# Performance work log

Hardware: AMD Instinct MI355X
Metric: run time of the kernel (lower is better)

## Reference

```python
import jax, jax.numpy as jnp
import numpy as np


def _pairwise_sqdist(a, b):
    # a: [B,N,2], b: [B,M,2] -> [B,N,M] squared Euclidean distances
    a2 = jnp.sum(a * a, axis=-1)  # [B,N]
    b2 = jnp.sum(b * b, axis=-1)  # [B,M]
    ab = jnp.einsum('bnd,bmd->bnm', a, b)  # [B,N,M]
    return a2[:, :, None] + b2[:, None, :] - 2.0 * ab


def setup_inputs() -> dict:
    key = jax.random.key(0)
    k1, k2 = jax.random.split(key)
    B, N, M, D = 16, 2048, 2048, 2
    preds = jax.random.normal(k1, (B, N, D), dtype=jnp.float32)
    targs = jax.random.normal(k2, (B, M, D), dtype=jnp.float32)
    subcoef = jnp.ones((D,), dtype=jnp.float32)
    return {"preds": preds, "targs": targs, "subcoef": subcoef}


def reference(preds, targs, subcoef):
    # Bidirectional Chamfer-style NN L1 loss, faithful to NNLoss.nn_loss.
    d2 = _pairwise_sqdist(preds, targs)  # [B,N,M]

    # preds -> nearest GT (KDTree over targs queried with preds)
    nn_t = jnp.argmin(d2, axis=2)  # [B,N]
    matched_t = jnp.take_along_axis(targs, nn_t[:, :, None], axis=1)  # [B,N,2]
    move_preds_to_gt = jnp.sum(jnp.abs(preds - matched_t) * subcoef)

    # targs -> nearest pred (KDTree over preds queried with targs)
    nn_p = jnp.argmin(d2, axis=1)  # [B,M]
    matched_p = jnp.take_along_axis(preds, nn_p[:, :, None], axis=1)  # [B,M,2]
    move_gts_to_pred = jnp.sum(jnp.abs(matched_p - targs))

    return move_gts_to_pred + move_preds_to_gt
```

## Files before the change

kernel.cpp:

```cpp
#include <hip/hip_runtime.h>


typedef float v2f __attribute__((ext_vector_type(2)));
typedef float v4f __attribute__((ext_vector_type(4)));

constexpr int B      = 16;
constexpr int NPTS   = 2048;
constexpr int BLK    = 1024;
constexpr int G      = 256;
constexpr int S      = 16;
constexpr int QPT    = 4;
constexpr int SEGLEN = NPTS / S;
constexpr int QUADS  = SEGLEN / 4;
constexpr int NBLK   = 2 * B * (NPTS / G);

__global__ __launch_bounds__(BLK) void nn_main(
    const float* __restrict__ preds, const float* __restrict__ targs,
    const float* __restrict__ subcoef, float* __restrict__ out)
{
    __shared__ v4f xs4[NPTS / 4];
    __shared__ v4f ys4[NPTS / 4];
    __shared__ unsigned long long cand[S * G];
    __shared__ float ssum[BLK / 64];

    const int blk  = blockIdx.x;
    const int dir  = blk >> 7;
    const int b    = (blk >> 3) & 15;
    const int tile = blk & 7;

    const float2* qb = reinterpret_cast<const float2*>(dir == 0 ? preds : targs)
                       + b * NPTS + tile * G;
    const float2* db = reinterpret_cast<const float2*>(dir == 0 ? targs : preds)
                       + b * NPTS;

    const float4* db4 = reinterpret_cast<const float4*>(db);
    {
        const int j = threadIdx.x & 511;
        const float4 a = db4[2 * j];
        const float4 c = db4[2 * j + 1];
        if (threadIdx.x < 512) xs4[j] = {a.x, a.z, c.x, c.z};
        else                   ys4[j] = {a.y, a.w, c.y, c.w};
    }

    const int qslot = threadIdx.x & 63;
    const int seg   = threadIdx.x >> 6;

    v2f   m2x[QPT], m2y[QPT];
    float best[QPT];
    int   bj[QPT];
    #pragma unroll
    for (int q = 0; q < QPT; ++q) {
        const float2 qp = qb[qslot + q * 64];
        const float ax = -2.0f * qp.x, ay = -2.0f * qp.y;
        m2x[q] = {ax, ax};
        m2y[q] = {ay, ay};
        best[q] = 3.402823466e+38f;
        bj[q] = 0;
    }
    __syncthreads();

    const v4f* xsp = xs4 + seg * QUADS;
    const v4f* ysp = ys4 + seg * QUADS;
    #pragma unroll 8
    for (int i = 0; i < QUADS; ++i) {
        const v4f X = xsp[i];
        const v4f Y = ysp[i];
        const v2f xa = {X.x, X.y}, xb = {X.z, X.w};
        const v2f ya = {Y.x, Y.y}, yb = {Y.z, Y.w};
        const v2f t2a = __builtin_elementwise_fma(xa, xa, ya * ya);
        const v2f t2b = __builtin_elementwise_fma(xb, xb, yb * yb);
        #pragma unroll
        for (int q = 0; q < QPT; ++q) {
            const v2f da = __builtin_elementwise_fma(
                m2x[q], xa, __builtin_elementwise_fma(m2y[q], ya, t2a));
            const v2f dc = __builtin_elementwise_fma(
                m2x[q], xb, __builtin_elementwise_fma(m2y[q], yb, t2b));
            const v2f m2 = __builtin_elementwise_min(da, dc);
            const float dm = fminf(m2.x, m2.y);
            if (dm < best[q]) { best[q] = dm; bj[q] = i; }
        }
    }

    #pragma unroll
    for (int q = 0; q < QPT; ++q) {
        const v4f X = xsp[bj[q]];
        const v4f Y = ysp[bj[q]];
        const v2f xa = {X.x, X.y}, xb = {X.z, X.w};
        const v2f ya = {Y.x, Y.y}, yb = {Y.z, Y.w};
        const v2f t2a = __builtin_elementwise_fma(xa, xa, ya * ya);
        const v2f t2b = __builtin_elementwise_fma(xb, xb, yb * yb);
        const v2f da = __builtin_elementwise_fma(
            m2x[q], xa, __builtin_elementwise_fma(m2y[q], ya, t2a));
        const v2f dc = __builtin_elementwise_fma(
            m2x[q], xb, __builtin_elementwise_fma(m2y[q], yb, t2b));
        int off = 3;
        if (dc.x == best[q]) off = 2;
        if (da.y == best[q]) off = 1;
        if (da.x == best[q]) off = 0;
        const int idx = seg * SEGLEN + 4 * bj[q] + off;
        unsigned int fb = __float_as_uint(best[q]);
        fb ^= 0x80000000u | (unsigned int)((int)fb >> 31);
        cand[seg * G + qslot + q * 64] =
            ((unsigned long long)fb << 32) | (unsigned int)idx;
    }
    __syncthreads();

    float val = 0.0f;
    if (threadIdx.x < G) {
        unsigned long long bp = cand[threadIdx.x];
        #pragma unroll
        for (int s = 1; s < S; ++s) {
            const unsigned long long v = cand[s * G + threadIdx.x];
            bp = v < bp ? v : bp;
        }
        const int idx = (int)(unsigned int)bp;
        const float2 qp = qb[threadIdx.x];
        const float2 tp = db[idx];
        float sx = 1.0f, sy = 1.0f;
        if (dir == 0) { sx = subcoef[0]; sy = subcoef[1]; }
        val = fabsf(qp.x - tp.x) * sx + fabsf(qp.y - tp.y) * sy;
    }

    #pragma unroll
    for (int off = 32; off > 0; off >>= 1)
        val += __shfl_down(val, off, 64);
    if ((threadIdx.x & 63) == 0) ssum[threadIdx.x >> 6] = val;
    __syncthreads();
    if (threadIdx.x == 0) {
        float s = ssum[0];
        #pragma unroll
        for (int w = 1; w < BLK / 64; ++w) s += ssum[w];
        atomicAdd(out, s);
    }
}

extern "C" void kernel_launch(void* const* d_in, const int* in_sizes, int n_in,
                              void* d_out, int out_size, void* d_ws, size_t ws_size,
                              hipStream_t stream) {
    const float* preds   = (const float*)d_in[0];
    const float* targs   = (const float*)d_in[1];
    const float* subcoef = (const float*)d_in[2];
    float* out = (float*)d_out;

    nn_main<<<NBLK, BLK, 0, stream>>>(preds, targs, subcoef, out);
}
```

Measured before the change: 73.61 us.

## Replace brute-force NN search with x-bucketed sort and pruned expanding scan

Adds a pre-pass kernel that bins each point set into 128 fixed-width x buckets via a shared-memory counting sort, storing records with their original indices. The main kernel then scans only the buckets covering a wavefront's query x-range, widening left or right while the bucket-edge lower bound can still beat the current best distance. This replaces the all-pairs distance scan with a pruned search. The costs are a second launch, a dependent pass through workspace memory, and possible wavefront divergence. The fixed bucket range [-5,5] is tuned to roughly normal inputs, and ties are broken by original index in the packed key.

```diff
diff --git a/kernel.cpp b/kernel.cpp
--- a/kernel.cpp
+++ b/kernel.cpp
@@ -2,135 +2,166 @@
 
 
 typedef float v2f __attribute__((ext_vector_type(2)));
-typedef float v4f __attribute__((ext_vector_type(4)));
 
-constexpr int B      = 16;
-constexpr int NPTS   = 2048;
-constexpr int BLK    = 1024;
-constexpr int G      = 256;
-constexpr int S      = 16;
-constexpr int QPT    = 4;
-constexpr int SEGLEN = NPTS / S;
-constexpr int QUADS  = SEGLEN / 4;
-constexpr int NBLK   = 2 * B * (NPTS / G);
+constexpr int   NPTS = 2048;
+constexpr int   NB   = 128;
+constexpr float XMIN = -5.0f;
+constexpr float BW   = 0.078125f;
+constexpr float INVW = 12.8f;
+constexpr float SLCK = 1e-5f;
 
-__global__ __launch_bounds__(BLK) void nn_main(
+constexpr size_t RECS_OFF  = 0;
+constexpr size_t START_OFF = 32 * NPTS * 16;
+
+__device__ __forceinline__ int xbucket(float x) {
+    int bk = (int)((x - XMIN) * INVW);
+    return bk < 0 ? 0 : (bk > NB - 1 ? NB - 1 : bk);
+}
+
+__device__ __forceinline__ unsigned long long shflx64(unsigned long long v, int m) {
+    unsigned int lo = (unsigned int)v, hi = (unsigned int)(v >> 32);
+    lo = __shfl_xor(lo, m, 64);
+    hi = __shfl_xor(hi, m, 64);
+    return ((unsigned long long)hi << 32) | lo;
+}
+
+__global__ __launch_bounds__(1024) void build_sorted(
     const float* __restrict__ preds, const float* __restrict__ targs,
-    const float* __restrict__ subcoef, float* __restrict__ out)
+    float4* __restrict__ recs, int* __restrict__ gstart)
 {
-    __shared__ v4f xs4[NPTS / 4];
-    __shared__ v4f ys4[NPTS / 4];
-    __shared__ unsigned long long cand[S * G];
-    __shared__ float ssum[BLK / 64];
+    __shared__ int cnt[NB];
+    __shared__ int ofs[NB];
+    __shared__ int wtot;
 
-    const int blk  = blockIdx.x;
-    const int dir  = blk >> 7;
-    const int b    = (blk >> 3) & 15;
-    const int tile = blk & 7;
+    const int s   = blockIdx.x;
+    const int t   = s >> 4;
+    const int b   = s & 15;
+    const int tid = threadIdx.x;
+    const float* src = (t == 0 ? preds : targs) + b * (NPTS * 2);
 
-    const float2* qb = reinterpret_cast<const float2*>(dir == 0 ? preds : targs)
-                       + b * NPTS + tile * G;
-    const float2* db = reinterpret_cast<const float2*>(dir == 0 ? targs : preds)
-                       + b * NPTS;
-
-    const float4* db4 = reinterpret_cast<const float4*>(db);
-    {
-        const int j = threadIdx.x & 511;
-        const float4 a = db4[2 * j];
-        const float4 c = db4[2 * j + 1];
-        if (threadIdx.x < 512) xs4[j] = {a.x, a.z, c.x, c.z};
-        else                   ys4[j] = {a.y, a.w, c.y, c.w};
-    }
-
-    const int qslot = threadIdx.x & 63;
-    const int seg   = threadIdx.x >> 6;
-
-    v2f   m2x[QPT], m2y[QPT];
-    float best[QPT];
-    int   bj[QPT];
-    #pragma unroll
-    for (int q = 0; q < QPT; ++q) {
-        const float2 qp = qb[qslot + q * 64];
-        const float ax = -2.0f * qp.x, ay = -2.0f * qp.y;
-        m2x[q] = {ax, ax};
-        m2y[q] = {ay, ay};
-        best[q] = 3.402823466e+38f;
-        bj[q] = 0;
-    }
+    if (tid < NB) cnt[tid] = 0;
     __syncthreads();
 
-    const v4f* xsp = xs4 + seg * QUADS;
-    const v4f* ysp = ys4 + seg * QUADS;
-    #pragma unroll 8
-    for (int i = 0; i < QUADS; ++i) {
-        const v4f X = xsp[i];
-        const v4f Y = ysp[i];
-        const v2f xa = {X.x, X.y}, xb = {X.z, X.w};
-        const v2f ya = {Y.x, Y.y}, yb = {Y.z, Y.w};
-        const v2f t2a = __builtin_elementwise_fma(xa, xa, ya * ya);
-        const v2f t2b = __builtin_elementwise_fma(xb, xb, yb * yb);
-        #pragma unroll
-        for (int q = 0; q < QPT; ++q) {
-            const v2f da = __builtin_elementwise_fma(
-                m2x[q], xa, __builtin_elementwise_fma(m2y[q], ya, t2a));
-            const v2f dc = __builtin_elementwise_fma(
-                m2x[q], xb, __builtin_elementwise_fma(m2y[q], yb, t2b));
-            const v2f m2 = __builtin_elementwise_min(da, dc);
-            const float dm = fminf(m2.x, m2.y);
-            if (dm < best[q]) { best[q] = dm; bj[q] = i; }
-        }
-    }
-
-    #pragma unroll
-    for (int q = 0; q < QPT; ++q) {
-        const v4f X = xsp[bj[q]];
-        const v4f Y = ysp[bj[q]];
-        const v2f xa = {X.x, X.y}, xb = {X.z, X.w};
-        const v2f ya = {Y.x, Y.y}, yb = {Y.z, Y.w};
-        const v2f t2a = __builtin_elementwise_fma(xa, xa, ya * ya);
-        const v2f t2b = __builtin_elementwise_fma(xb, xb, yb * yb);
-        const v2f da = __builtin_elementwise_fma(
-            m2x[q], xa, __builtin_elementwise_fma(m2y[q], ya, t2a));
-        const v2f dc = __builtin_elementwise_fma(
-            m2x[q], xb, __builtin_elementwise_fma(m2y[q], yb, t2b));
-        int off = 3;
-        if (dc.x == best[q]) off = 2;
-        if (da.y == best[q]) off = 1;
-        if (da.x == best[q]) off = 0;
-        const int idx = seg * SEGLEN + 4 * bj[q] + off;
-        unsigned int fb = __float_as_uint(best[q]);
-        fb ^= 0x80000000u | (unsigned int)((int)fb >> 31);
-        cand[seg * G + qslot + q * 64] =
-            ((unsigned long long)fb << 32) | (unsigned int)idx;
-    }
+    const float4 f = reinterpret_cast<const float4*>(src)[tid];
+    const int bk0 = xbucket(f.x);
+    const int bk1 = xbucket(f.z);
+    atomicAdd(&cnt[bk0], 1);
+    atomicAdd(&cnt[bk1], 1);
     __syncthreads();
 
+    const int lane = tid & 63;
+    int v = (tid < NB) ? cnt[tid] : 0;
+    #pragma unroll
+    for (int off = 1; off < 64; off <<= 1) {
+        const int u = __shfl_up(v, off, 64);
+        if (lane >= off) v += u;
+    }
+    if (tid == 63) wtot = v;
+    __syncthreads();
+    if (tid >= 64 && tid < NB) v += wtot;
+    if (tid < NB) {
+        const int ex = v - cnt[tid];
+        ofs[tid] = ex;
+        gstart[s * (NB + 1) + tid] = ex;
+    }
+    if (tid == 0) gstart[s * (NB + 1) + NB] = NPTS;
+    __syncthreads();
+
+    {
+        const int p0 = atomicAdd(&ofs[bk0], 1);
+        recs[s * NPTS + p0] = {f.x, f.y, __int_as_float(2 * tid), 0.0f};
+        const int p1 = atomicAdd(&ofs[bk1], 1);
+        recs[s * NPTS + p1] = {f.z, f.w, __int_as_float(2 * tid + 1), 0.0f};
+    }
+}
+
+__global__ __launch_bounds__(256) void nn_pruned(
+    const float* __restrict__ preds, const float* __restrict__ targs,
+    const float* __restrict__ subcoef, float* __restrict__ out,
+    const float4* __restrict__ recs, const int* __restrict__ gstart)
+{
+    __shared__ int   st[NB + 1];
+    __shared__ float ssum[4];
+
+    const int blk = blockIdx.x;
+    const int tid = threadIdx.x;
+    const int dir  = blk >> 9;
+    const int b    = (blk >> 5) & 15;
+    const int tile = blk & 31;
+
+    const int qset = (dir ? 16 : 0) + b;
+    const int dset = (dir ? 0 : 16) + b;
+
+    if (tid <= NB) st[tid] = gstart[dset * (NB + 1) + tid];
+    __syncthreads();
+
+    const int qs  = tile * 64 + (tid >> 2);
+    const int sub = tid & 3;
+    const float4 qr = recs[qset * NPTS + qs];
+    const float qx = qr.x, qy = qr.y;
+
+    float xmn = qx, xmx = qx;
+    #pragma unroll
+    for (int m = 1; m < 64; m <<= 1) {
+        xmn = fminf(xmn, __shfl_xor(xmn, m, 64));
+        xmx = fmaxf(xmx, __shfl_xor(xmx, m, 64));
+    }
+    int blo = xbucket(xmn);
+    int bhi = xbucket(xmx);
+
+    const float4* P = recs + dset * NPTS;
+    unsigned long long best = 0x7F800000FFFFFFFFull;
+
+    int jlo = st[blo];
+    int jhi = st[bhi + 1];
+
+    #define SCAN(a, bnd)                                                        \
+        for (int j = (a) + sub; j < (bnd); j += 4) {                            \
+            const float4 r = P[j];                                              \
+            const float dx = qx - r.x, dy = qy - r.y;                           \
+            const float d2 = fmaf(dx, dx, dy * dy);                             \
+            const unsigned long long pk =                                       \
+                ((unsigned long long)__float_as_uint(d2) << 32) |               \
+                (unsigned int)__float_as_int(r.z);                              \
+            best = pk < best ? pk : best;                                       \
+        }
+
+    SCAN(jlo, jhi)
+
+    while (true) {
+        unsigned long long o = shflx64(best, 1); best = o < best ? o : best;
+        o = shflx64(best, 2);                    best = o < best ? o : best;
+        const float bd = __uint_as_float((unsigned int)(best >> 32));
+        const float lb = fmaxf(qx - fmaf((float)blo, BW, XMIN) - SLCK, 0.0f);
+        const float rb = fmaxf(fmaf((float)(bhi + 1), BW, XMIN) - qx - SLCK, 0.0f);
+        const bool nl = (blo > 0)      && (lb * lb <= bd);
+        const bool nr = (bhi < NB - 1) && (rb * rb <= bd);
+        const bool aL = __any(nl), aR = __any(nr);
+        if (!aL && !aR) break;
+        if (aL) { --blo; const int a = st[blo];      SCAN(a, jlo)   jlo = a; }
+        if (aR) { ++bhi; const int e = st[bhi + 1];  SCAN(jhi, e)   jhi = e; }
+    }
+    #undef SCAN
+
     float val = 0.0f;
-    if (threadIdx.x < G) {
-        unsigned long long bp = cand[threadIdx.x];
-        #pragma unroll
-        for (int s = 1; s < S; ++s) {
-            const unsigned long long v = cand[s * G + threadIdx.x];
-            bp = v < bp ? v : bp;
-        }
-        const int idx = (int)(unsigned int)bp;
-        const float2 qp = qb[threadIdx.x];
-        const float2 tp = db[idx];
+    if (sub == 0) {
+        const int idx = (int)(unsigned int)best;
+        const float2* dbo = reinterpret_cast<const float2*>(dir ? preds : targs)
+                            + b * NPTS;
+        const float2 tp = dbo[idx];
         float sx = 1.0f, sy = 1.0f;
         if (dir == 0) { sx = subcoef[0]; sy = subcoef[1]; }
-        val = fabsf(qp.x - tp.x) * sx + fabsf(qp.y - tp.y) * sy;
+        val = fabsf(qx - tp.x) * sx + fabsf(qy - tp.y) * sy;
     }
 
     #pragma unroll
     for (int off = 32; off > 0; off >>= 1)
         val += __shfl_down(val, off, 64);
-    if ((threadIdx.x & 63) == 0) ssum[threadIdx.x >> 6] = val;
+    if ((tid & 63) == 0) ssum[tid >> 6] = val;
     __syncthreads();
-    if (threadIdx.x == 0) {
-        float s = ssum[0];
-        #pragma unroll
-        for (int w = 1; w < BLK / 64; ++w) s += ssum[w];
-        atomicAdd(out, s);
+    if (tid == 0) {
+        const float s2 = ssum[0] + ssum[1] + ssum[2] + ssum[3];
+        atomicAdd(out, s2);
     }
 }
 
@@ -142,5 +173,9 @@
     const float* subcoef = (const float*)d_in[2];
     float* out = (float*)d_out;
 
-    nn_main<<<NBLK, BLK, 0, stream>>>(preds, targs, subcoef, out);
+    float4* recs = (float4*)((char*)d_ws + RECS_OFF);
+    int*    gst  = (int*)((char*)d_ws + START_OFF);
+
+    build_sorted<<<32, 1024, 0, stream>>>(preds, targs, recs, gst);
+    nn_pruned<<<1024, 256, 0, stream>>>(preds, targs, subcoef, out, recs, gst);
 }
```

After: 119.0 us. +61.7%, slower.
